# Optimization experiments

Hardware: AMD Instinct MI355X
Metric: run time of the kernel (lower is better)

The kernel has to match this reference:

```python
import jax, jax.numpy as jnp
import numpy as np

PLACEHOLDER = -1
B, S, V = 128, 8, 32000  # batch, spec tokens per request, vocab
T = B * S


def setup_inputs() -> dict:
    key = jax.random.key(0)
    ks = jax.random.split(key, 8)
    target_logits = jax.random.normal(ks[0], (T, V), dtype=jnp.float32)
    dp = jax.random.uniform(ks[1], (T, V), dtype=jnp.float32)
    draft_probs = dp / jnp.sum(dp, axis=-1, keepdims=True)  # valid prob dist per token
    draft_token_ids = jax.random.randint(ks[2], (T,), 0, V, dtype=jnp.int32)
    bonus_token_ids = jax.random.randint(ks[3], (B,), 0, V, dtype=jnp.int32)
    temperature = 0.5 + jax.random.uniform(ks[4], (B,), dtype=jnp.float32)  # >0 => all random
    uniform_probs = jax.random.uniform(ks[5], (T,), dtype=jnp.float32)
    # q ~ Exponential(1), as torch's q.exponential_()
    u = jax.random.uniform(ks[6], (B, V), dtype=jnp.float32, minval=1e-10, maxval=1.0)
    q = -jnp.log(u)
    cu_num_draft_tokens = (jnp.arange(B, dtype=jnp.int32) + 1) * S
    return {
        'target_logits': target_logits,
        'draft_probs': draft_probs,
        'draft_token_ids': draft_token_ids,
        'bonus_token_ids': bonus_token_ids,
        'temperature': temperature,
        'uniform_probs': uniform_probs,
        'q': q,
        'cu_num_draft_tokens': cu_num_draft_tokens,
    }


def reference(target_logits, draft_probs, draft_token_ids, bonus_token_ids,
              temperature, uniform_probs, q, cu_num_draft_tokens):
    # compute_probs: softmax of logits / per-token expanded temperature
    temp_tok = jnp.repeat(temperature, S)  # [T]
    target_probs = jax.nn.softmax(target_logits / temp_tok[:, None], axis=-1)  # [T, V]

    tok = jnp.arange(T)
    req = tok // S  # request index per token (uniform raggedness)

    # accept/reject: target_prob/draft_prob >= u  (guard draft_prob > 0)
    p_tgt = target_probs[tok, draft_token_ids]  # [T]
    p_drf = draft_probs[tok, draft_token_ids]   # [T]
    accept = (p_drf > 0) & (p_tgt >= uniform_probs * p_drf)  # [T]

    # recovered tokens: argmax(max(p_tgt - p_drf, 0) / q) over vocab (Gumbel-max trick)
    resid = jnp.maximum(target_probs - draft_probs, 0.0)  # [T, V]
    recovered = jnp.argmax(resid / q[req], axis=-1).astype(jnp.int32)  # [T]

    # sequential accept until first rejection, then placeholder; bonus if all accepted
    accept_b = accept.reshape(B, S)
    alive = jnp.concatenate(
        [jnp.ones((B, 1), dtype=bool),
         jnp.cumprod(accept_b[:, :-1].astype(jnp.int32), axis=1).astype(bool)],
        axis=1)  # alive[b, p] = all accepts before pos p
    tok_out = jnp.where(accept_b, draft_token_ids.reshape(B, S), recovered.reshape(B, S))
    main = jnp.where(alive, tok_out, PLACEHOLDER)  # [B, S]
    all_acc = jnp.all(accept_b, axis=1)
    bonus_col = jnp.where(all_acc, bonus_token_ids, PLACEHOLDER)  # [B]
    output_token_ids = jnp.concatenate([main, bonus_col[:, None]], axis=1)  # [B, S+1]
    return output_token_ids
```

## Files before the change

kernel.cpp:

```cpp
#include <hip/hip_runtime.h>


constexpr int PLACEHOLDER = -1;
constexpr int B = 128;
constexpr int S = 8;
constexpr int V = 32000;
constexpr int NV4 = V / 4;

extern "C" __device__ float __builtin_amdgcn_exp2f(float);
extern "C" __device__ float __builtin_amdgcn_rcpf(float);

__global__ __launch_bounds__(1024, 4)
void rs_seq(const float* __restrict__ logits,
            const float* __restrict__ dprobs,
            const float* __restrict__ q,
            const int*   __restrict__ draft_ids,
            const int*   __restrict__ bonus_ids,
            const float* __restrict__ temperature,
            const float* __restrict__ uniform_probs,
            int* __restrict__ out)
{
    const int b   = blockIdx.x;
    const int tid = threadIdx.x, lane = tid & 63, wid = tid >> 6;
    __shared__ float s_red[16];
    __shared__ float s_ld[S], s_dd[S], s_u[S];
    __shared__ int   s_dt[S];
    __shared__ int   s_bonus;
    __shared__ float s_D;
    __shared__ int   s_dec;
    __shared__ float s_val[16];
    __shared__ int   s_idx[16];

    const float c = 1.4426950408889634f / temperature[b];

    if (wid == 0) {
        if (lane < S) {
            const int t  = b * S + lane;
            const int dt = draft_ids[t];
            s_dt[lane] = dt;
            s_u[lane]  = uniform_probs[t];
            s_ld[lane] = logits[(size_t)t * V + dt];
            s_dd[lane] = dprobs[(size_t)t * V + dt];
        }
        if (lane == 8) s_bonus = bonus_ids[b];
    }

    float4 cur[8], nxt[8];
    {
        const float4* lrow = (const float4*)(logits + (size_t)(b * S) * V);
        #pragma unroll
        for (int j = 0; j < 8; ++j) {
            const int i4 = j * 1024 + tid;
            if (i4 < NV4) cur[j] = lrow[i4];
        }
    }

    int   need_p = S;
    float Dsave  = 0.f;

    for (int p = 0; p < S; ++p) {
        if (p + 1 < S) {
            const float4* lrn =
                (const float4*)(logits + (size_t)(b * S + p + 1) * V);
            #pragma unroll
            for (int j = 0; j < 8; ++j) {
                const int i4 = j * 1024 + tid;
                if (i4 < NV4) nxt[j] = lrn[i4];
            }
        }
        float lsum = 0.f;
        #pragma unroll
        for (int j = 0; j < 8; ++j) {
            const int i4 = j * 1024 + tid;
            if (i4 < NV4) {
                const float4 v = cur[j];
                lsum += (__builtin_amdgcn_exp2f(v.x * c) +
                         __builtin_amdgcn_exp2f(v.y * c)) +
                        (__builtin_amdgcn_exp2f(v.z * c) +
                         __builtin_amdgcn_exp2f(v.w * c));
            }
        }
        #pragma unroll
        for (int off = 32; off >= 1; off >>= 1)
            lsum += __shfl_xor(lsum, off, 64);
        if (lane == 0) s_red[wid] = lsum;
        __syncthreads();
        if (tid == 0) {
            float D = 0.f;
            #pragma unroll
            for (int w = 0; w < 16; ++w) D += s_red[w];
            const float e_d = __builtin_amdgcn_exp2f(s_ld[p] * c);
            s_dec = (s_dd[p] > 0.f) && (e_d >= s_u[p] * s_dd[p] * D);
            s_D   = D;
        }
        __syncthreads();
        if (!s_dec) { need_p = p; Dsave = s_D; break; }
        #pragma unroll
        for (int j = 0; j < 8; ++j) cur[j] = nxt[j];
    }

    if (need_p >= S) {
        if (tid < S) out[b * (S + 1) + tid] = s_dt[tid];
        if (tid == 0) out[b * (S + 1) + S] = s_bonus;
        return;
    }

    const int   t = b * S + need_p;
    const float D = Dsave;
    const float4* drow = (const float4*)(dprobs + (size_t)t * V);
    const float4* qrow = (const float4*)(q      + (size_t)b * V);

    float bestv = -__builtin_inff();
    int   besti = 0x7fffffff;

#define RS_COMP(LC, DC, QC, GIDX)                                          \
    {                                                                      \
        const float e  = __builtin_amdgcn_exp2f((LC) * c);                 \
        const float rq = __builtin_amdgcn_rcpf(QC);                        \
        const float r  = fmaf(-((DC) * rq), D, e * rq);                    \
        if (r > bestv) { bestv = r; besti = (GIDX); }                      \
    }

    #pragma unroll
    for (int ph = 0; ph < 2; ++ph) {
        float4 dv[4], qv[4];
        #pragma unroll
        for (int j = 0; j < 4; ++j) {
            const int i4 = (ph * 4 + j) * 1024 + tid;
            if (i4 < NV4) dv[j] = drow[i4];
        }
        #pragma unroll
        for (int j = 0; j < 4; ++j) {
            const int i4 = (ph * 4 + j) * 1024 + tid;
            if (i4 < NV4) qv[j] = qrow[i4];
        }
        #pragma unroll
        for (int j = 0; j < 4; ++j) {
            const int jj = ph * 4 + j;
            const int i4 = jj * 1024 + tid;
            if (i4 < NV4) {
                const float4 lv = cur[jj];
                const int base  = i4 * 4;
                RS_COMP(lv.x, dv[j].x, qv[j].x, base + 0)
                RS_COMP(lv.y, dv[j].y, qv[j].y, base + 1)
                RS_COMP(lv.z, dv[j].z, qv[j].z, base + 2)
                RS_COMP(lv.w, dv[j].w, qv[j].w, base + 3)
            }
        }
    }
#undef RS_COMP

    #pragma unroll
    for (int off = 32; off >= 1; off >>= 1) {
        const float ov = __shfl_xor(bestv, off, 64);
        const int   oi = __shfl_xor(besti, off, 64);
        if (ov > bestv || (ov == bestv && oi < besti)) { bestv = ov; besti = oi; }
    }
    if (lane == 0) { s_val[wid] = bestv; s_idx[wid] = besti; }
    __syncthreads();
    if (wid == 0) {
        float bv = (lane < 16) ? s_val[lane] : -__builtin_inff();
        int   bi = (lane < 16) ? s_idx[lane] : 0x7fffffff;
        #pragma unroll
        for (int off = 8; off >= 1; off >>= 1) {
            const float ov = __shfl_xor(bv, off, 64);
            const int   oi = __shfl_xor(bi, off, 64);
            if (ov > bv || (ov == bv && oi < bi)) { bv = ov; bi = oi; }
        }
        if (lane == 0) {
            #pragma unroll
            for (int p = 0; p < S; ++p) {
                int tok = PLACEHOLDER;
                if (p < need_p)       tok = s_dt[p];
                else if (p == need_p) tok = bi;
                out[b * (S + 1) + p] = tok;
            }
            out[b * (S + 1) + S] = PLACEHOLDER;
        }
    }
}

extern "C" void kernel_launch(void* const* d_in, const int* in_sizes, int n_in,
                              void* d_out, int out_size, void* d_ws, size_t ws_size,
                              hipStream_t stream) {
    const float* logits      = (const float*)d_in[0];
    const float* dprobs      = (const float*)d_in[1];
    const int*   draft_ids   = (const int*)d_in[2];
    const int*   bonus_ids   = (const int*)d_in[3];
    const float* temperature = (const float*)d_in[4];
    const float* uniform     = (const float*)d_in[5];
    const float* q           = (const float*)d_in[6];

    int* out = (int*)d_out;
    rs_seq<<<B, 1024, 0, stream>>>(logits, dprobs, q, draft_ids, bonus_ids,
                                   temperature, uniform, out);
}
```

Before: 31.79 us.

## Prefetch two logits rows ahead and replace second barrier with redundant reduction

The sequential accept walk now keeps two register buffers of logit rows and prefetches row p+2 while row p is processed, so loads run further ahead. Every thread sums the per-wave partials itself from alternating shared arrays, which removes the second barrier and the shared decision broadcast in each step. The residual argmax phase reloads the rejected logits row from memory instead of reusing registers. The cost is higher register pressure, extra memory reads, and 16 redundant shared-memory reads per thread per step.

```diff
diff --git a/kernel.cpp b/kernel.cpp
--- a/kernel.cpp
+++ b/kernel.cpp
@@ -22,12 +22,10 @@
 {
     const int b   = blockIdx.x;
     const int tid = threadIdx.x, lane = tid & 63, wid = tid >> 6;
-    __shared__ float s_red[16];
+    __shared__ float s_redA[16], s_redB[16];
     __shared__ float s_ld[S], s_dd[S], s_u[S];
     __shared__ int   s_dt[S];
     __shared__ int   s_bonus;
-    __shared__ float s_D;
-    __shared__ int   s_dec;
     __shared__ float s_val[16];
     __shared__ int   s_idx[16];
 
@@ -45,137 +43,152 @@
         if (lane == 8) s_bonus = bonus_ids[b];
     }
 
-    float4 cur[8], nxt[8];
-    {
-        const float4* lrow = (const float4*)(logits + (size_t)(b * S) * V);
-        #pragma unroll
-        for (int j = 0; j < 8; ++j) {
-            const int i4 = j * 1024 + tid;
-            if (i4 < NV4) cur[j] = lrow[i4];
-        }
+    const float4* lbase = (const float4*)(logits + (size_t)(b * S) * V);
+
+    float4 bufA[8], bufB[8];
+    #pragma unroll
+    for (int j = 0; j < 8; ++j) {
+        const int i4 = j * 1024 + tid;
+        if (i4 < NV4) bufA[j] = lbase[i4];
+    }
+    #pragma unroll
+    for (int j = 0; j < 8; ++j) {
+        const int i4 = j * 1024 + tid;
+        if (i4 < NV4) bufB[j] = lbase[NV4 + i4];
     }
 
     int   need_p = S;
     float Dsave  = 0.f;
 
-    for (int p = 0; p < S; ++p) {
-        if (p + 1 < S) {
-            const float4* lrn =
-                (const float4*)(logits + (size_t)(b * S + p + 1) * V);
-            #pragma unroll
-            for (int j = 0; j < 8; ++j) {
-                const int i4 = j * 1024 + tid;
-                if (i4 < NV4) nxt[j] = lrn[i4];
-            }
-        }
-        float lsum = 0.f;
-        #pragma unroll
-        for (int j = 0; j < 8; ++j) {
-            const int i4 = j * 1024 + tid;
-            if (i4 < NV4) {
-                const float4 v = cur[j];
-                lsum += (__builtin_amdgcn_exp2f(v.x * c) +
-                         __builtin_amdgcn_exp2f(v.y * c)) +
-                        (__builtin_amdgcn_exp2f(v.z * c) +
-                         __builtin_amdgcn_exp2f(v.w * c));
-            }
-        }
-        #pragma unroll
-        for (int off = 32; off >= 1; off >>= 1)
-            lsum += __shfl_xor(lsum, off, 64);
-        if (lane == 0) s_red[wid] = lsum;
-        __syncthreads();
-        if (tid == 0) {
-            float D = 0.f;
-            #pragma unroll
-            for (int w = 0; w < 16; ++w) D += s_red[w];
-            const float e_d = __builtin_amdgcn_exp2f(s_ld[p] * c);
-            s_dec = (s_dd[p] > 0.f) && (e_d >= s_u[p] * s_dd[p] * D);
-            s_D   = D;
-        }
-        __syncthreads();
-        if (!s_dec) { need_p = p; Dsave = s_D; break; }
-        #pragma unroll
-        for (int j = 0; j < 8; ++j) cur[j] = nxt[j];
-    }
-
+#define WALK_STEP(P, BUF, SRED)                                             \
+    {                                                                       \
+        float lsum = 0.f;                                                   \
+        _Pragma("unroll")                                                   \
+        for (int j = 0; j < 8; ++j) {                                       \
+            const int i4 = j * 1024 + tid;                                  \
+            if (i4 < NV4) {                                                 \
+                const float4 v = BUF[j];                                    \
+                lsum += (__builtin_amdgcn_exp2f(v.x * c) +                  \
+                         __builtin_amdgcn_exp2f(v.y * c)) +                 \
+                        (__builtin_amdgcn_exp2f(v.z * c) +                  \
+                         __builtin_amdgcn_exp2f(v.w * c));                  \
+            }                                                               \
+        }                                                                   \
+        if ((P) + 2 < S) {                                                  \
+            _Pragma("unroll")                                               \
+            for (int j = 0; j < 8; ++j) {                                   \
+                const int i4 = j * 1024 + tid;                              \
+                if (i4 < NV4) BUF[j] = lbase[((P) + 2) * NV4 + i4];         \
+            }                                                               \
+        }                                                                   \
+        _Pragma("unroll")                                                   \
+        for (int off = 32; off >= 1; off >>= 1)                             \
+            lsum += __shfl_xor(lsum, off, 64);                              \
+        if (lane == 0) SRED[wid] = lsum;                                    \
+        __syncthreads();                                                    \
+        float D = 0.f;                                                      \
+        _Pragma("unroll")                                                   \
+        for (int w = 0; w < 16; ++w) D += SRED[w];                          \
+        const float e_d = __builtin_amdgcn_exp2f(s_ld[(P)] * c);            \
+        const bool dec = (s_dd[(P)] > 0.f) &&                               \
+                         (e_d >= s_u[(P)] * s_dd[(P)] * D);                 \
+        if (!dec) { need_p = (P); Dsave = D; goto walk_done; }              \
+    }
+
+    WALK_STEP(0, bufA, s_redA)
+    WALK_STEP(1, bufB, s_redB)
+    WALK_STEP(2, bufA, s_redA)
+    WALK_STEP(3, bufB, s_redB)
+    WALK_STEP(4, bufA, s_redA)
+    WALK_STEP(5, bufB, s_redB)
+    WALK_STEP(6, bufA, s_redA)
+    WALK_STEP(7, bufB, s_redB)
+#undef WALK_STEP
+
+walk_done:
     if (need_p >= S) {
         if (tid < S) out[b * (S + 1) + tid] = s_dt[tid];
         if (tid == 0) out[b * (S + 1) + S] = s_bonus;
         return;
     }
 
-    const int   t = b * S + need_p;
-    const float D = Dsave;
-    const float4* drow = (const float4*)(dprobs + (size_t)t * V);
-    const float4* qrow = (const float4*)(q      + (size_t)b * V);
-
-    float bestv = -__builtin_inff();
-    int   besti = 0x7fffffff;
+    {
+        const int   t = b * S + need_p;
+        const float D = Dsave;
+        const float4* lrow = (const float4*)(logits + (size_t)t * V);
+        const float4* drow = (const float4*)(dprobs + (size_t)t * V);
+        const float4* qrow = (const float4*)(q      + (size_t)b * V);
+
+        float bestv = -__builtin_inff();
+        int   besti = 0x7fffffff;
 
 #define RS_COMP(LC, DC, QC, GIDX)                                          \
-    {                                                                      \
-        const float e  = __builtin_amdgcn_exp2f((LC) * c);                 \
-        const float rq = __builtin_amdgcn_rcpf(QC);                        \
-        const float r  = fmaf(-((DC) * rq), D, e * rq);                    \
-        if (r > bestv) { bestv = r; besti = (GIDX); }                      \
-    }
-
-    #pragma unroll
-    for (int ph = 0; ph < 2; ++ph) {
-        float4 dv[4], qv[4];
+        {                                                                  \
+            const float e  = __builtin_amdgcn_exp2f((LC) * c);             \
+            const float rq = __builtin_amdgcn_rcpf(QC);                    \
+            const float r  = fmaf(-((DC) * rq), D, e * rq);                \
+            if (r > bestv) { bestv = r; besti = (GIDX); }                  \
+        }
+
         #pragma unroll
-        for (int j = 0; j < 4; ++j) {
-            const int i4 = (ph * 4 + j) * 1024 + tid;
-            if (i4 < NV4) dv[j] = drow[i4];
-        }
+        for (int ph = 0; ph < 2; ++ph) {
+            float4 lv[4], dv[4], qv[4];
+            #pragma unroll
+            for (int j = 0; j < 4; ++j) {
+                const int i4 = (ph * 4 + j) * 1024 + tid;
+                if (i4 < NV4) lv[j] = lrow[i4];
+            }
+            #pragma unroll
+            for (int j = 0; j < 4; ++j) {
+                const int i4 = (ph * 4 + j) * 1024 + tid;
+                if (i4 < NV4) dv[j] = drow[i4];
+            }
+            #pragma unroll
+            for (int j = 0; j < 4; ++j) {
+                const int i4 = (ph * 4 + j) * 1024 + tid;
+                if (i4 < NV4) qv[j] = qrow[i4];
+            }
+            #pragma unroll
+            for (int j = 0; j < 4; ++j) {
+                const int i4 = (ph * 4 + j) * 1024 + tid;
+                if (i4 < NV4) {
+                    const int base = i4 * 4;
+                    RS_COMP(lv[j].x, dv[j].x, qv[j].x, base + 0)
+                    RS_COMP(lv[j].y, dv[j].y, qv[j].y, base + 1)
+                    RS_COMP(lv[j].z, dv[j].z, qv[j].z, base + 2)
+                    RS_COMP(lv[j].w, dv[j].w, qv[j].w, base + 3)
+                }
+            }
+        }
+#undef RS_COMP
+
         #pragma unroll
-        for (int j = 0; j < 4; ++j) {
-            const int i4 = (ph * 4 + j) * 1024 + tid;
-            if (i4 < NV4) qv[j] = qrow[i4];
-        }
-        #pragma unroll
-        for (int j = 0; j < 4; ++j) {
-            const int jj = ph * 4 + j;
-            const int i4 = jj * 1024 + tid;
-            if (i4 < NV4) {
-                const float4 lv = cur[jj];
-                const int base  = i4 * 4;
-                RS_COMP(lv.x, dv[j].x, qv[j].x, base + 0)
-                RS_COMP(lv.y, dv[j].y, qv[j].y, base + 1)
-                RS_COMP(lv.z, dv[j].z, qv[j].z, base + 2)
-                RS_COMP(lv.w, dv[j].w, qv[j].w, base + 3)
-            }
-        }
-    }
-#undef RS_COMP
-
-    #pragma unroll
-    for (int off = 32; off >= 1; off >>= 1) {
-        const float ov = __shfl_xor(bestv, off, 64);
-        const int   oi = __shfl_xor(besti, off, 64);
-        if (ov > bestv || (ov == bestv && oi < besti)) { bestv = ov; besti = oi; }
-    }
-    if (lane == 0) { s_val[wid] = bestv; s_idx[wid] = besti; }
-    __syncthreads();
-    if (wid == 0) {
-        float bv = (lane < 16) ? s_val[lane] : -__builtin_inff();
-        int   bi = (lane < 16) ? s_idx[lane] : 0x7fffffff;
-        #pragma unroll
-        for (int off = 8; off >= 1; off >>= 1) {
-            const float ov = __shfl_xor(bv, off, 64);
-            const int   oi = __shfl_xor(bi, off, 64);
-            if (ov > bv || (ov == bv && oi < bi)) { bv = ov; bi = oi; }
-        }
-        if (lane == 0) {
-            #pragma unroll
-            for (int p = 0; p < S; ++p) {
-                int tok = PLACEHOLDER;
-                if (p < need_p)       tok = s_dt[p];
-                else if (p == need_p) tok = bi;
-                out[b * (S + 1) + p] = tok;
-            }
-            out[b * (S + 1) + S] = PLACEHOLDER;
+        for (int off = 32; off >= 1; off >>= 1) {
+            const float ov = __shfl_xor(bestv, off, 64);
+            const int   oi = __shfl_xor(besti, off, 64);
+            if (ov > bestv || (ov == bestv && oi < besti)) { bestv = ov; besti = oi; }
+        }
+        if (lane == 0) { s_val[wid] = bestv; s_idx[wid] = besti; }
+        __syncthreads();
+        if (wid == 0) {
+            float bv = (lane < 16) ? s_val[lane] : -__builtin_inff();
+            int   bi = (lane < 16) ? s_idx[lane] : 0x7fffffff;
+            #pragma unroll
+            for (int off = 8; off >= 1; off >>= 1) {
+                const float ov = __shfl_xor(bv, off, 64);
+                const int   oi = __shfl_xor(bi, off, 64);
+                if (ov > bv || (ov == bv && oi < bi)) { bv = ov; bi = oi; }
+            }
+            if (lane == 0) {
+                #pragma unroll
+                for (int p = 0; p < S; ++p) {
+                    int tok = PLACEHOLDER;
+                    if (p < need_p)       tok = s_dt[p];
+                    else if (p == need_p) tok = bi;
+                    out[b * (S + 1) + p] = tok;
+                }
+                out[b * (S + 1) + S] = PLACEHOLDER;
+            }
         }
     }
 }
```

Result: faster. 30.64 us, median of 2 (-3.6%).
